# Optimization experiments

Hardware: AMD Instinct MI355X
Metric: run time of the kernel (lower is better)

## Reference

```python
import jax, jax.numpy as jnp
import numpy as np

EPS = 1e-5      # eps used in abs() and log()
BN_EPS = 1e-5   # torch BatchNorm2d default eps


def setup_inputs() -> dict:
    key = jax.random.key(0)
    ks = jax.random.split(key, 5)
    N, C, F, T = 16, 4, 257, 1000
    B, K = 8, 80
    xr = jax.random.normal(ks[0], (N, C, F, T), dtype=jnp.float32)
    xi = jax.random.normal(ks[1], (N, C, F, T), dtype=jnp.float32)
    # per-bin complex beamforming weights: (F, B, C) == Conv1d weight (B*F, 1, C) regrouped
    wr = jax.random.normal(ks[2], (F, B, C), dtype=jnp.float32) * 0.25
    wi = jax.random.normal(ks[3], (F, B, C), dtype=jnp.float32) * 0.25
    # nn.Linear(num_bins, spectra_filters, bias=False) weight: (K, F)
    w_proj = jax.random.normal(ks[4], (K, F), dtype=jnp.float32) * (1.0 / np.sqrt(F))
    gamma = jnp.ones((B,), dtype=jnp.float32)
    beta = jnp.zeros((B,), dtype=jnp.float32)
    return {"xr": xr, "xi": xi, "wr": wr, "wi": wi, "w_proj": w_proj,
            "gamma": gamma, "beta": beta}


def reference(xr, xi, wr, wi, w_proj, gamma, beta):
    # Grouped complex conv1d == per-bin complex beamform across mics:
    # out[n,b,t,f] = sum_c w[f,b,c] * x[n,c,f,t] (complex product)
    br = jnp.einsum('ncft,fbc->nbtf', xr, wr) - jnp.einsum('ncft,fbc->nbtf', xi, wi)
    bi = jnp.einsum('ncft,fbc->nbtf', xi, wr) + jnp.einsum('ncft,fbc->nbtf', xr, wi)
    mag = jnp.sqrt(br * br + bi * bi + EPS)              # (N, B, T, F)
    # Linear(F -> K), ReLU, log
    f = jax.nn.relu(jnp.einsum('nbtf,kf->nbtk', mag, w_proj))
    f = jnp.log(f + EPS)                                  # (N, B, T, K)
    # BatchNorm2d over channel axis B (training-mode batch statistics)
    mean = jnp.mean(f, axis=(0, 2, 3), keepdims=True)
    var = jnp.var(f, axis=(0, 2, 3), keepdims=True)
    f = (f - mean) * jax.lax.rsqrt(var + BN_EPS)
    f = f * gamma[None, :, None, None] + beta[None, :, None, None]
    N, B, T, K = f.shape
    # (N, B, T, K) -> (N, T, B*K)
    return jnp.transpose(f, (0, 2, 1, 3)).reshape(N, T, B * K)
```

## Files before the change

kernel.cpp:

```cpp
#include <hip/hip_runtime.h>
#include <math.h>

#define N_ 16
#define C_ 4
#define F_ 257
#define T_ 1000
#define TP_ 1024
#define B_ 8
#define K_ 80
#define BK_ (B_*K_)

static __device__ __forceinline__ float relu_log(float v) {
    v = fmaxf(v, 0.0f);
    return logf(v + 1e-5f);
}

__global__ __launch_bounds__(256) void k_beamform(
    const float* __restrict__ xr, const float* __restrict__ xi,
    const float* __restrict__ wr, const float* __restrict__ wi,
    float* __restrict__ mag) {
    const int blk = blockIdx.x;
    const int f = blk % F_;
    const int n = blk / F_;

    float wrr[B_][C_], wii[B_][C_];
#pragma unroll
    for (int b = 0; b < B_; ++b)
#pragma unroll
        for (int c = 0; c < C_; ++c) {
            wrr[b][c] = wr[(f * B_ + b) * C_ + c];
            wii[b][c] = wi[(f * B_ + b) * C_ + c];
        }

    const float* xr0 = xr + (size_t)n * C_ * F_ * T_ + (size_t)f * T_;
    const float* xi0 = xi + (size_t)n * C_ * F_ * T_ + (size_t)f * T_;
    float* mag0 = mag + ((size_t)(n * B_) * F_ + f) * TP_;

    for (int t = threadIdx.x; t < TP_; t += 256) {
        if (t < T_) {
            float xrv[C_], xiv[C_];
#pragma unroll
            for (int c = 0; c < C_; ++c) {
                xrv[c] = xr0[(size_t)c * F_ * T_ + t];
                xiv[c] = xi0[(size_t)c * F_ * T_ + t];
            }
#pragma unroll
            for (int b = 0; b < B_; ++b) {
                float br = 0.f, bi = 0.f;
#pragma unroll
                for (int c = 0; c < C_; ++c) {
                    br += xrv[c] * wrr[b][c];
                    br -= xiv[c] * wii[b][c];
                    bi += xiv[c] * wrr[b][c];
                    bi += xrv[c] * wii[b][c];
                }
                float m = sqrtf(br * br + bi * bi + 1e-5f);
                mag0[(size_t)b * F_ * TP_ + t] = m;
            }
        } else {
#pragma unroll
            for (int b = 0; b < B_; ++b)
                mag0[(size_t)b * F_ * TP_ + t] = 0.f;
        }
    }
}

__global__ __launch_bounds__(256) void k_proj(
    const float* __restrict__ mag, const float* __restrict__ w_proj,
    float* __restrict__ out, double* __restrict__ sums) {
    const int bid = blockIdx.x;
    const int tt = bid & 15;
    const int b = (bid >> 4) & 7;
    const int n = bid >> 7;
    const int t0 = tt * 64;

    const int tid = threadIdx.x;
    const int kx = tid & 15;
    const int ty = tid >> 4;
    const int kb = kx * 5;

    __shared__ float magS[32][64];
    __shared__ float wS[32][81];

    float acc[5][4];
#pragma unroll
    for (int j = 0; j < 5; ++j)
#pragma unroll
        for (int i = 0; i < 4; ++i) acc[j][i] = 0.f;

    const float* magNB = mag + ((size_t)(n * B_ + b) * F_) * TP_;

    for (int ch = 0; ch < 8; ++ch) {
        const int f0 = ch * 32;
#pragma unroll
        for (int r = 0; r < 2; ++r) {
            int idx = tid + r * 256;
            int row = idx >> 4, c4 = idx & 15;
            float4 v = *(const float4*)(magNB + (size_t)(f0 + row) * TP_ + t0 + c4 * 4);
            *(float4*)&magS[row][c4 * 4] = v;
        }
#pragma unroll
        for (int r = 0; r < 10; ++r) {
            int idx = tid + r * 256;
            int k = idx >> 5, fc = idx & 31;
            wS[fc][k] = w_proj[k * F_ + f0 + fc];
        }
        __syncthreads();
#pragma unroll 8
        for (int fc = 0; fc < 32; ++fc) {
            float4 m = *(const float4*)&magS[fc][ty * 4];
#pragma unroll
            for (int j = 0; j < 5; ++j) {
                float w = wS[fc][kb + j];
                acc[j][0] += w * m.x;
                acc[j][1] += w * m.y;
                acc[j][2] += w * m.z;
                acc[j][3] += w * m.w;
            }
        }
        __syncthreads();
    }
    {
        float4 m = *(const float4*)(magNB + (size_t)256 * TP_ + t0 + ty * 4);
#pragma unroll
        for (int j = 0; j < 5; ++j) {
            float w = w_proj[(kb + j) * F_ + 256];
            acc[j][0] += w * m.x;
            acc[j][1] += w * m.y;
            acc[j][2] += w * m.z;
            acc[j][3] += w * m.w;
        }
    }

    double s1 = 0.0, s2 = 0.0;
#pragma unroll
    for (int i = 0; i < 4; ++i) {
        int t = t0 + ty * 4 + i;
        if (t < T_) {
            float* orow = out + ((size_t)n * T_ + t) * BK_ + b * K_ + kb;
#pragma unroll
            for (int j = 0; j < 5; ++j) {
                float v = relu_log(acc[j][i]);
                orow[j] = v;
                s1 += (double)v;
                s2 += (double)v * (double)v;
            }
        }
    }
#pragma unroll
    for (int off = 32; off; off >>= 1) {
        s1 += __shfl_down(s1, off);
        s2 += __shfl_down(s2, off);
    }
    __shared__ double red1[4], red2[4];
    int wid = tid >> 6, lane = tid & 63;
    if (lane == 0) { red1[wid] = s1; red2[wid] = s2; }
    __syncthreads();
    if (tid == 0) {
        double a1 = red1[0] + red1[1] + red1[2] + red1[3];
        double a2 = red2[0] + red2[1] + red2[2] + red2[3];
        atomicAdd(&sums[b], a1);
        atomicAdd(&sums[B_ + b], a2);
    }
}

__global__ void k_bnstats(const double* __restrict__ sums,
                          const float* __restrict__ gamma,
                          const float* __restrict__ beta,
                          float* __restrict__ ss) {
    int b = threadIdx.x;
    if (b < B_) {
        const double cnt = (double)N_ * T_ * K_;
        double mean = sums[b] / cnt;
        double var = sums[B_ + b] / cnt - mean * mean;
        float scale = gamma[b] * (float)(1.0 / sqrt(var + 1e-5));
        float shift = beta[b] - (float)mean * scale;
        ss[b] = scale;
        ss[B_ + b] = shift;
    }
}

__global__ __launch_bounds__(256) void k_bnapply(float* __restrict__ out,
                                                 const float* __restrict__ ss) {
    size_t i4 = (size_t)blockIdx.x * 256 + threadIdx.x;
    int k4 = (int)(i4 % (BK_ / 4));
    int b = k4 / (K_ / 4);
    float scale = ss[b], shift = ss[B_ + b];
    float4* p = (float4*)out + i4;
    float4 v = *p;
    v.x = v.x * scale + shift;
    v.y = v.y * scale + shift;
    v.z = v.z * scale + shift;
    v.w = v.w * scale + shift;
    *p = v;
}

extern "C" void kernel_launch(void* const* d_in, const int* in_sizes, int n_in,
                              void* d_out, int out_size, void* d_ws, size_t ws_size,
                              hipStream_t stream) {
    const float* xr = (const float*)d_in[0];
    const float* xi = (const float*)d_in[1];
    const float* wr = (const float*)d_in[2];
    const float* wi = (const float*)d_in[3];
    const float* w_proj = (const float*)d_in[4];
    const float* gamma = (const float*)d_in[5];
    const float* beta = (const float*)d_in[6];
    float* out = (float*)d_out;

    double* sums = (double*)d_ws;
    float* ss = (float*)((char*)d_ws + 128);
    float* mag = (float*)((char*)d_ws + 512);

    hipMemsetAsync(d_ws, 0, 512, stream);
    k_beamform<<<N_ * F_, 256, 0, stream>>>(xr, xi, wr, wi, mag);
    k_proj<<<N_ * B_ * 16, 256, 0, stream>>>(mag, w_proj, out, sums);
    k_bnstats<<<1, 64, 0, stream>>>(sums, gamma, beta, ss);
    k_bnapply<<<10000, 256, 0, stream>>>(out, ss);
}
```

Before: 166.7 us.

## Fuse beamforming into projection kernel, computing magnitudes directly into shared memory

Merges the beamform and projection kernels so each block computes its per-bin magnitudes from the raw complex inputs straight into shared memory, removing the large intermediate magnitude buffer in global memory. The time tile grows to 128 with an 8x5 register tile per thread. The cost is that input spectra are re-read once per beam channel, relying on cache hits, and the grid shrinks, which may lower occupancy.

After: 196.8 us. +18.1%, slower.

```diff
diff --git a/kernel.cpp b/kernel.cpp
--- a/kernel.cpp
+++ b/kernel.cpp
@@ -5,139 +5,162 @@
 #define C_ 4
 #define F_ 257
 #define T_ 1000
-#define TP_ 1024
 #define B_ 8
 #define K_ 80
 #define BK_ (B_*K_)
+#define TT_ 128
 
 static __device__ __forceinline__ float relu_log(float v) {
     v = fmaxf(v, 0.0f);
     return logf(v + 1e-5f);
 }
 
-__global__ __launch_bounds__(256) void k_beamform(
+__global__ __launch_bounds__(256, 4) void k_fused(
     const float* __restrict__ xr, const float* __restrict__ xi,
     const float* __restrict__ wr, const float* __restrict__ wi,
-    float* __restrict__ mag) {
-    const int blk = blockIdx.x;
-    const int f = blk % F_;
-    const int n = blk / F_;
-
-    float wrr[B_][C_], wii[B_][C_];
-#pragma unroll
-    for (int b = 0; b < B_; ++b)
-#pragma unroll
-        for (int c = 0; c < C_; ++c) {
-            wrr[b][c] = wr[(f * B_ + b) * C_ + c];
-            wii[b][c] = wi[(f * B_ + b) * C_ + c];
-        }
-
-    const float* xr0 = xr + (size_t)n * C_ * F_ * T_ + (size_t)f * T_;
-    const float* xi0 = xi + (size_t)n * C_ * F_ * T_ + (size_t)f * T_;
-    float* mag0 = mag + ((size_t)(n * B_) * F_ + f) * TP_;
-
-    for (int t = threadIdx.x; t < TP_; t += 256) {
-        if (t < T_) {
-            float xrv[C_], xiv[C_];
-#pragma unroll
-            for (int c = 0; c < C_; ++c) {
-                xrv[c] = xr0[(size_t)c * F_ * T_ + t];
-                xiv[c] = xi0[(size_t)c * F_ * T_ + t];
-            }
-#pragma unroll
-            for (int b = 0; b < B_; ++b) {
-                float br = 0.f, bi = 0.f;
-#pragma unroll
-                for (int c = 0; c < C_; ++c) {
-                    br += xrv[c] * wrr[b][c];
-                    br -= xiv[c] * wii[b][c];
-                    bi += xiv[c] * wrr[b][c];
-                    bi += xrv[c] * wii[b][c];
-                }
-                float m = sqrtf(br * br + bi * bi + 1e-5f);
-                mag0[(size_t)b * F_ * TP_ + t] = m;
-            }
-        } else {
-#pragma unroll
-            for (int b = 0; b < B_; ++b)
-                mag0[(size_t)b * F_ * TP_ + t] = 0.f;
-        }
-    }
-}
-
-__global__ __launch_bounds__(256) void k_proj(
-    const float* __restrict__ mag, const float* __restrict__ w_proj,
+    const float* __restrict__ w_proj,
     float* __restrict__ out, double* __restrict__ sums) {
+
+    const int tid = threadIdx.x;
     const int bid = blockIdx.x;
-    const int tt = bid & 15;
-    const int b = (bid >> 4) & 7;
-    const int n = bid >> 7;
-    const int t0 = tt * 64;
-
-    const int tid = threadIdx.x;
+    const int b  = bid & 7;
+    const int tt = (bid >> 3) & 7;
+    const int n  = bid >> 6;
+    const int t0 = tt * TT_;
+
+    __shared__ float magS[32][TT_];
+    __shared__ float wS[32][TT_];
+
     const int kx = tid & 15;
     const int ty = tid >> 4;
-    const int kb = kx * 5;
-
-    __shared__ float magS[32][64];
-    __shared__ float wS[32][81];
-
-    float acc[5][4];
+
+    float acc[5][8];
 #pragma unroll
     for (int j = 0; j < 5; ++j)
 #pragma unroll
-        for (int i = 0; i < 4; ++i) acc[j][i] = 0.f;
-
-    const float* magNB = mag + ((size_t)(n * B_ + b) * F_) * TP_;
+        for (int i = 0; i < 8; ++i) acc[j][i] = 0.f;
+
+    const float* xrn = xr + (size_t)n * C_ * F_ * T_;
+    const float* xin = xi + (size_t)n * C_ * F_ * T_;
 
     for (int ch = 0; ch < 8; ++ch) {
         const int f0 = ch * 32;
-#pragma unroll
-        for (int r = 0; r < 2; ++r) {
-            int idx = tid + r * 256;
-            int row = idx >> 4, c4 = idx & 15;
-            float4 v = *(const float4*)(magNB + (size_t)(f0 + row) * TP_ + t0 + c4 * 4);
-            *(float4*)&magS[row][c4 * 4] = v;
-        }
 #pragma unroll
         for (int r = 0; r < 10; ++r) {
             int idx = tid + r * 256;
             int k = idx >> 5, fc = idx & 31;
-            wS[fc][k] = w_proj[k * F_ + f0 + fc];
+            wS[fc][(k / 5) * 8 + (k % 5)] = w_proj[k * F_ + f0 + fc];
+        }
+#pragma unroll
+        for (int r = 0; r < 4; ++r) {
+            int idx = tid + r * 256;
+            int fr = idx >> 5, t4 = idx & 31;
+            int f = f0 + fr;
+            int tb = t0 + t4 * 4;
+            if (tb < T_) {
+                float xrv[C_][4], xiv[C_][4];
+#pragma unroll
+                for (int c = 0; c < C_; ++c) {
+                    float4 vr = *(const float4*)(xrn + ((size_t)c * F_ + f) * T_ + tb);
+                    float4 vi = *(const float4*)(xin + ((size_t)c * F_ + f) * T_ + tb);
+                    xrv[c][0] = vr.x; xrv[c][1] = vr.y; xrv[c][2] = vr.z; xrv[c][3] = vr.w;
+                    xiv[c][0] = vi.x; xiv[c][1] = vi.y; xiv[c][2] = vi.z; xiv[c][3] = vi.w;
+                }
+                float4 wrv = *(const float4*)(wr + (size_t)(f * B_ + b) * C_);
+                float4 wiv = *(const float4*)(wi + (size_t)(f * B_ + b) * C_);
+                float wrc[4] = {wrv.x, wrv.y, wrv.z, wrv.w};
+                float wic[4] = {wiv.x, wiv.y, wiv.z, wiv.w};
+                float4 mres;
+                float* mp = &mres.x;
+#pragma unroll
+                for (int i = 0; i < 4; ++i) {
+                    float br = 0.f, bim = 0.f;
+#pragma unroll
+                    for (int c = 0; c < C_; ++c) {
+                        br  += xrv[c][i] * wrc[c] - xiv[c][i] * wic[c];
+                        bim += xiv[c][i] * wrc[c] + xrv[c][i] * wic[c];
+                    }
+                    mp[i] = sqrtf(br * br + bim * bim + 1e-5f);
+                }
+                *(float4*)&magS[fr][t4 * 4] = mres;
+            } else {
+                *(float4*)&magS[fr][t4 * 4] = make_float4(0.f, 0.f, 0.f, 0.f);
+            }
         }
         __syncthreads();
-#pragma unroll 8
+#pragma unroll 4
         for (int fc = 0; fc < 32; ++fc) {
-            float4 m = *(const float4*)&magS[fc][ty * 4];
-#pragma unroll
-            for (int j = 0; j < 5; ++j) {
-                float w = wS[fc][kb + j];
-                acc[j][0] += w * m.x;
-                acc[j][1] += w * m.y;
-                acc[j][2] += w * m.z;
-                acc[j][3] += w * m.w;
-            }
+            float4 m0 = *(const float4*)&magS[fc][ty * 8];
+            float4 m1 = *(const float4*)&magS[fc][ty * 8 + 4];
+            float4 w0 = *(const float4*)&wS[fc][kx * 8];
+            float  w4 = wS[fc][kx * 8 + 4];
+            float wj[5] = {w0.x, w0.y, w0.z, w0.w, w4};
+            float mi[8] = {m0.x, m0.y, m0.z, m0.w, m1.x, m1.y, m1.z, m1.w};
+#pragma unroll
+            for (int j = 0; j < 5; ++j)
+#pragma unroll
+                for (int i = 0; i < 8; ++i)
+                    acc[j][i] += wj[j] * mi[i];
         }
         __syncthreads();
     }
+
+    if (tid < 80)
+        wS[0][(tid / 5) * 8 + (tid % 5)] = w_proj[tid * F_ + 256];
+    if (tid >= 128 && tid < 160) {
+        int t4 = tid - 128;
+        int tb = t0 + t4 * 4;
+        if (tb < T_) {
+            float xrv[C_][4], xiv[C_][4];
+#pragma unroll
+            for (int c = 0; c < C_; ++c) {
+                float4 vr = *(const float4*)(xrn + ((size_t)c * F_ + 256) * T_ + tb);
+                float4 vi = *(const float4*)(xin + ((size_t)c * F_ + 256) * T_ + tb);
+                xrv[c][0] = vr.x; xrv[c][1] = vr.y; xrv[c][2] = vr.z; xrv[c][3] = vr.w;
+                xiv[c][0] = vi.x; xiv[c][1] = vi.y; xiv[c][2] = vi.z; xiv[c][3] = vi.w;
+            }
+            float4 wrv = *(const float4*)(wr + (size_t)(256 * B_ + b) * C_);
+            float4 wiv = *(const float4*)(wi + (size_t)(256 * B_ + b) * C_);
+            float wrc[4] = {wrv.x, wrv.y, wrv.z, wrv.w};
+            float wic[4] = {wiv.x, wiv.y, wiv.z, wiv.w};
+            float4 mres;
+            float* mp = &mres.x;
+#pragma unroll
+            for (int i = 0; i < 4; ++i) {
+                float br = 0.f, bim = 0.f;
+#pragma unroll
+                for (int c = 0; c < C_; ++c) {
+                    br  += xrv[c][i] * wrc[c] - xiv[c][i] * wic[c];
+                    bim += xiv[c][i] * wrc[c] + xrv[c][i] * wic[c];
+                }
+                mp[i] = sqrtf(br * br + bim * bim + 1e-5f);
+            }
+            *(float4*)&magS[0][t4 * 4] = mres;
+        } else {
+            *(float4*)&magS[0][t4 * 4] = make_float4(0.f, 0.f, 0.f, 0.f);
+        }
+    }
+    __syncthreads();
     {
-        float4 m = *(const float4*)(magNB + (size_t)256 * TP_ + t0 + ty * 4);
-#pragma unroll
-        for (int j = 0; j < 5; ++j) {
-            float w = w_proj[(kb + j) * F_ + 256];
-            acc[j][0] += w * m.x;
-            acc[j][1] += w * m.y;
-            acc[j][2] += w * m.z;
-            acc[j][3] += w * m.w;
-        }
+        float4 m0 = *(const float4*)&magS[0][ty * 8];
+        float4 m1 = *(const float4*)&magS[0][ty * 8 + 4];
+        float4 w0 = *(const float4*)&wS[0][kx * 8];
+        float  w4 = wS[0][kx * 8 + 4];
+        float wj[5] = {w0.x, w0.y, w0.z, w0.w, w4};
+        float mi[8] = {m0.x, m0.y, m0.z, m0.w, m1.x, m1.y, m1.z, m1.w};
+#pragma unroll
+        for (int j = 0; j < 5; ++j)
+#pragma unroll
+            for (int i = 0; i < 8; ++i)
+                acc[j][i] += wj[j] * mi[i];
     }
 
     double s1 = 0.0, s2 = 0.0;
 #pragma unroll
-    for (int i = 0; i < 4; ++i) {
-        int t = t0 + ty * 4 + i;
+    for (int i = 0; i < 8; ++i) {
+        int t = t0 + ty * 8 + i;
         if (t < T_) {
-            float* orow = out + ((size_t)n * T_ + t) * BK_ + b * K_ + kb;
+            float* orow = out + ((size_t)n * T_ + t) * BK_ + b * K_ + kx * 5;
 #pragma unroll
             for (int j = 0; j < 5; ++j) {
                 float v = relu_log(acc[j][i]);
@@ -209,11 +232,9 @@
 
     double* sums = (double*)d_ws;
     float* ss = (float*)((char*)d_ws + 128);
-    float* mag = (float*)((char*)d_ws + 512);
 
     hipMemsetAsync(d_ws, 0, 512, stream);
-    k_beamform<<<N_ * F_, 256, 0, stream>>>(xr, xi, wr, wi, mag);
-    k_proj<<<N_ * B_ * 16, 256, 0, stream>>>(mag, w_proj, out, sums);
+    k_fused<<<N_ * B_ * 8, 256, 0, stream>>>(xr, xi, wr, wi, w_proj, out, sums);
     k_bnstats<<<1, 64, 0, stream>>>(sums, gamma, beta, ss);
     k_bnapply<<<10000, 256, 0, stream>>>(out, ss);
 }
```

## Fuse beamforming into projection kernel and replace atomics with per-block partials

Applied to the files above, without the earlier changes.

Beamforming magnitudes are now computed per 16-frame tile directly into shared memory inside the projection kernel, so the large intermediate magnitude buffer is never written to or read back from global memory. Each block handles all 8 beams for one (n, time-tile), accumulating an 8x5 register tile per thread. BN statistics are written as per-block partial sums reduced by a wider stats kernel, which removes the memset and the double atomics. The cost is that each block recomputes beamforming across all frequencies and holds more registers, and the small 16-frame tiles give lower reuse of the projection weights.

Result: no change. 168.8 us (+1.2%).

```diff
diff --git a/kernel.cpp b/kernel.cpp
--- a/kernel.cpp
+++ b/kernel.cpp
@@ -5,174 +5,224 @@
 #define C_ 4
 #define F_ 257
 #define T_ 1000
-#define TP_ 1024
 #define B_ 8
 #define K_ 80
-#define BK_ (B_*K_)
+#define BK_ 640
+#define TT_ 16
+#define NT_ 63
+#define NBLK (N_ * NT_)
+#define MSTR 260
+#define WSTR 162
 
 static __device__ __forceinline__ float relu_log(float v) {
     v = fmaxf(v, 0.0f);
     return logf(v + 1e-5f);
 }
 
-__global__ __launch_bounds__(256) void k_beamform(
+__global__ __launch_bounds__(256, 3) void k_fused(
     const float* __restrict__ xr, const float* __restrict__ xi,
     const float* __restrict__ wr, const float* __restrict__ wi,
-    float* __restrict__ mag) {
-    const int blk = blockIdx.x;
-    const int f = blk % F_;
-    const int n = blk / F_;
-
-    float wrr[B_][C_], wii[B_][C_];
-#pragma unroll
-    for (int b = 0; b < B_; ++b)
-#pragma unroll
-        for (int c = 0; c < C_; ++c) {
-            wrr[b][c] = wr[(f * B_ + b) * C_ + c];
-            wii[b][c] = wi[(f * B_ + b) * C_ + c];
-        }
-
-    const float* xr0 = xr + (size_t)n * C_ * F_ * T_ + (size_t)f * T_;
-    const float* xi0 = xi + (size_t)n * C_ * F_ * T_ + (size_t)f * T_;
-    float* mag0 = mag + ((size_t)(n * B_) * F_ + f) * TP_;
-
-    for (int t = threadIdx.x; t < TP_; t += 256) {
-        if (t < T_) {
-            float xrv[C_], xiv[C_];
-#pragma unroll
-            for (int c = 0; c < C_; ++c) {
-                xrv[c] = xr0[(size_t)c * F_ * T_ + t];
-                xiv[c] = xi0[(size_t)c * F_ * T_ + t];
-            }
-#pragma unroll
-            for (int b = 0; b < B_; ++b) {
-                float br = 0.f, bi = 0.f;
-#pragma unroll
-                for (int c = 0; c < C_; ++c) {
-                    br += xrv[c] * wrr[b][c];
-                    br -= xiv[c] * wii[b][c];
-                    bi += xiv[c] * wrr[b][c];
-                    bi += xrv[c] * wii[b][c];
-                }
-                float m = sqrtf(br * br + bi * bi + 1e-5f);
-                mag0[(size_t)b * F_ * TP_ + t] = m;
-            }
-        } else {
-#pragma unroll
-            for (int b = 0; b < B_; ++b)
-                mag0[(size_t)b * F_ * TP_ + t] = 0.f;
-        }
-    }
-}
-
-__global__ __launch_bounds__(256) void k_proj(
-    const float* __restrict__ mag, const float* __restrict__ w_proj,
-    float* __restrict__ out, double* __restrict__ sums) {
+    const float* __restrict__ w_proj,
+    float* __restrict__ out, double* __restrict__ partials) {
+
+    const int tid = threadIdx.x;
     const int bid = blockIdx.x;
-    const int tt = bid & 15;
-    const int b = (bid >> 4) & 7;
-    const int n = bid >> 7;
-    const int t0 = tt * 64;
-
-    const int tid = threadIdx.x;
+    const int tt = bid % NT_;
+    const int n  = bid / NT_;
+    const int t0 = tt * TT_;
+
+    __shared__ float magS[TT_][MSTR];
+    __shared__ float wS[32][WSTR];
+    __shared__ double redS[2][4][B_];
+
     const int kx = tid & 15;
     const int ty = tid >> 4;
-    const int kb = kx * 5;
-
-    __shared__ float magS[32][64];
-    __shared__ float wS[32][81];
-
-    float acc[5][4];
-#pragma unroll
-    for (int j = 0; j < 5; ++j)
-#pragma unroll
-        for (int i = 0; i < 4; ++i) acc[j][i] = 0.f;
-
-    const float* magNB = mag + ((size_t)(n * B_ + b) * F_) * TP_;
+
+    const int m_bh = tid & 1;
+    const int m_t4 = (tid >> 1) & 3;
+    const int m_fr = tid >> 3;
+    const int m_b0 = m_bh * 4;
+
+    float acc[B_][5];
+#pragma unroll
+    for (int b = 0; b < B_; ++b)
+#pragma unroll
+        for (int j = 0; j < 5; ++j) acc[b][j] = 0.f;
+
+    const float* xrn = xr + (size_t)n * C_ * F_ * T_;
+    const float* xin = xi + (size_t)n * C_ * F_ * T_;
+    const int kbase = tid >> 5;
+    const int wfc   = tid & 31;
 
     for (int ch = 0; ch < 8; ++ch) {
         const int f0 = ch * 32;
 #pragma unroll
-        for (int r = 0; r < 2; ++r) {
-            int idx = tid + r * 256;
-            int row = idx >> 4, c4 = idx & 15;
-            float4 v = *(const float4*)(magNB + (size_t)(f0 + row) * TP_ + t0 + c4 * 4);
-            *(float4*)&magS[row][c4 * 4] = v;
-        }
-#pragma unroll
         for (int r = 0; r < 10; ++r) {
-            int idx = tid + r * 256;
-            int k = idx >> 5, fc = idx & 31;
-            wS[fc][k] = w_proj[k * F_ + f0 + fc];
+            int k = kbase + 8 * r;
+            wS[wfc][(k / 5) * 10 + (k % 5)] = w_proj[k * F_ + f0 + wfc];
+        }
+        {
+            const int f  = f0 + m_fr;
+            const int tb = t0 + m_t4 * 4;
+            float m[4][4];
+            if (tb + 4 <= T_) {
+                const float* xrp = xrn + (size_t)f * T_ + tb;
+                const float* xip = xin + (size_t)f * T_ + tb;
+                float xrv[C_][4], xiv[C_][4];
+#pragma unroll
+                for (int c = 0; c < C_; ++c) {
+                    float4 vr = *(const float4*)(xrp + (size_t)c * F_ * T_);
+                    float4 vi = *(const float4*)(xip + (size_t)c * F_ * T_);
+                    xrv[c][0] = vr.x; xrv[c][1] = vr.y; xrv[c][2] = vr.z; xrv[c][3] = vr.w;
+                    xiv[c][0] = vi.x; xiv[c][1] = vi.y; xiv[c][2] = vi.z; xiv[c][3] = vi.w;
+                }
+                const float* wrp = wr + (size_t)(f * B_ + m_b0) * C_;
+                const float* wip = wi + (size_t)(f * B_ + m_b0) * C_;
+#pragma unroll
+                for (int jb = 0; jb < 4; ++jb) {
+                    float4 wrv = *(const float4*)(wrp + jb * C_);
+                    float4 wiv = *(const float4*)(wip + jb * C_);
+                    float wrc[4] = {wrv.x, wrv.y, wrv.z, wrv.w};
+                    float wic[4] = {wiv.x, wiv.y, wiv.z, wiv.w};
+#pragma unroll
+                    for (int i = 0; i < 4; ++i) {
+                        float br = 0.f, bi2 = 0.f;
+#pragma unroll
+                        for (int c = 0; c < C_; ++c) {
+                            br  += xrv[c][i] * wrc[c] - xiv[c][i] * wic[c];
+                            bi2 += xiv[c][i] * wrc[c] + xrv[c][i] * wic[c];
+                        }
+                        m[i][jb] = sqrtf(br * br + bi2 * bi2 + 1e-5f);
+                    }
+                }
+            } else {
+#pragma unroll
+                for (int i = 0; i < 4; ++i)
+#pragma unroll
+                    for (int jb = 0; jb < 4; ++jb) m[i][jb] = 0.f;
+            }
+#pragma unroll
+            for (int i = 0; i < 4; ++i)
+                *(float4*)&magS[m_t4 * 4 + i][m_fr * 8 + m_b0] =
+                    make_float4(m[i][0], m[i][1], m[i][2], m[i][3]);
         }
         __syncthreads();
 #pragma unroll 8
         for (int fc = 0; fc < 32; ++fc) {
-            float4 m = *(const float4*)&magS[fc][ty * 4];
+            float4 m0 = *(const float4*)&magS[ty][fc * 8];
+            float4 m1 = *(const float4*)&magS[ty][fc * 8 + 4];
+            float2 wa = *(const float2*)&wS[fc][kx * 10];
+            float2 wb = *(const float2*)&wS[fc][kx * 10 + 2];
+            float  w4 = wS[fc][kx * 10 + 4];
+            float wj[5] = {wa.x, wa.y, wb.x, wb.y, w4};
+            float mb[8] = {m0.x, m0.y, m0.z, m0.w, m1.x, m1.y, m1.z, m1.w};
+#pragma unroll
+            for (int b = 0; b < B_; ++b)
+#pragma unroll
+                for (int j = 0; j < 5; ++j)
+                    acc[b][j] += mb[b] * wj[j];
+        }
+        __syncthreads();
+    }
+
+    if (tid < 80)
+        wS[0][(tid / 5) * 10 + (tid % 5)] = w_proj[tid * F_ + 256];
+    if (tid >= 128) {
+        int id = tid - 128;
+        int trow = id >> 3;
+        int b = id & 7;
+        int t = t0 + trow;
+        float v = 0.f;
+        if (t < T_) {
+            const float* wrp = wr + (size_t)(256 * B_ + b) * C_;
+            const float* wip = wi + (size_t)(256 * B_ + b) * C_;
+            float br = 0.f, bi2 = 0.f;
+#pragma unroll
+            for (int c = 0; c < C_; ++c) {
+                float xrv = xrn[((size_t)c * F_ + 256) * T_ + t];
+                float xiv = xin[((size_t)c * F_ + 256) * T_ + t];
+                br  += xrv * wrp[c] - xiv * wip[c];
+                bi2 += xiv * wrp[c] + xrv * wip[c];
+            }
+            v = sqrtf(br * br + bi2 * bi2 + 1e-5f);
+        }
+        magS[trow][b] = v;
+    }
+    __syncthreads();
+    {
+        float4 m0 = *(const float4*)&magS[ty][0];
+        float4 m1 = *(const float4*)&magS[ty][4];
+        float2 wa = *(const float2*)&wS[0][kx * 10];
+        float2 wb = *(const float2*)&wS[0][kx * 10 + 2];
+        float  w4 = wS[0][kx * 10 + 4];
+        float wj[5] = {wa.x, wa.y, wb.x, wb.y, w4};
+        float mb[8] = {m0.x, m0.y, m0.z, m0.w, m1.x, m1.y, m1.z, m1.w};
+#pragma unroll
+        for (int b = 0; b < B_; ++b)
+#pragma unroll
+            for (int j = 0; j < 5; ++j)
+                acc[b][j] += mb[b] * wj[j];
+    }
+
+    float s1f[B_], s2f[B_];
+#pragma unroll
+    for (int b = 0; b < B_; ++b) { s1f[b] = 0.f; s2f[b] = 0.f; }
+    const int t = t0 + ty;
+    if (t < T_) {
+        float* orow = out + ((size_t)n * T_ + t) * BK_ + kx * 5;
+#pragma unroll
+        for (int b = 0; b < B_; ++b) {
 #pragma unroll
             for (int j = 0; j < 5; ++j) {
-                float w = wS[fc][kb + j];
-                acc[j][0] += w * m.x;
-                acc[j][1] += w * m.y;
-                acc[j][2] += w * m.z;
-                acc[j][3] += w * m.w;
+                float v = relu_log(acc[b][j]);
+                orow[b * K_ + j] = v;
+                s1f[b] += v;
+                s2f[b] += v * v;
             }
         }
-        __syncthreads();
-    }
-    {
-        float4 m = *(const float4*)(magNB + (size_t)256 * TP_ + t0 + ty * 4);
-#pragma unroll
-        for (int j = 0; j < 5; ++j) {
-            float w = w_proj[(kb + j) * F_ + 256];
-            acc[j][0] += w * m.x;
-            acc[j][1] += w * m.y;
-            acc[j][2] += w * m.z;
-            acc[j][3] += w * m.w;
-        }
-    }
-
+    }
+    const int wid = tid >> 6, lane = tid & 63;
+#pragma unroll
+    for (int b = 0; b < B_; ++b) {
+        double d1 = (double)s1f[b], d2 = (double)s2f[b];
+#pragma unroll
+        for (int off = 32; off; off >>= 1) {
+            d1 += __shfl_down(d1, off);
+            d2 += __shfl_down(d2, off);
+        }
+        if (lane == 0) { redS[0][wid][b] = d1; redS[1][wid][b] = d2; }
+    }
+    __syncthreads();
+    if (tid < 8) {
+        partials[(size_t)bid * 16 + tid] =
+            redS[0][0][tid] + redS[0][1][tid] + redS[0][2][tid] + redS[0][3][tid];
+    } else if (tid >= 64 && tid < 72) {
+        int b = tid - 64;
+        partials[(size_t)bid * 16 + 8 + b] =
+            redS[1][0][b] + redS[1][1][b] + redS[1][2][b] + redS[1][3][b];
+    }
+}
+
+__global__ __launch_bounds__(256) void k_bnstats(
+    const double* __restrict__ partials,
+    const float* __restrict__ gamma, const float* __restrict__ beta,
+    float* __restrict__ ss) {
+    const int b = threadIdx.x >> 5;
+    const int i = threadIdx.x & 31;
     double s1 = 0.0, s2 = 0.0;
-#pragma unroll
-    for (int i = 0; i < 4; ++i) {
-        int t = t0 + ty * 4 + i;
-        if (t < T_) {
-            float* orow = out + ((size_t)n * T_ + t) * BK_ + b * K_ + kb;
-#pragma unroll
-            for (int j = 0; j < 5; ++j) {
-                float v = relu_log(acc[j][i]);
-                orow[j] = v;
-                s1 += (double)v;
-                s2 += (double)v * (double)v;
-            }
-        }
-    }
-#pragma unroll
-    for (int off = 32; off; off >>= 1) {
+    for (int j = i; j < NBLK; j += 32) {
+        s1 += partials[(size_t)j * 16 + b];
+        s2 += partials[(size_t)j * 16 + 8 + b];
+    }
+#pragma unroll
+    for (int off = 16; off; off >>= 1) {
         s1 += __shfl_down(s1, off);
         s2 += __shfl_down(s2, off);
     }
-    __shared__ double red1[4], red2[4];
-    int wid = tid >> 6, lane = tid & 63;
-    if (lane == 0) { red1[wid] = s1; red2[wid] = s2; }
-    __syncthreads();
-    if (tid == 0) {
-        double a1 = red1[0] + red1[1] + red1[2] + red1[3];
-        double a2 = red2[0] + red2[1] + red2[2] + red2[3];
-        atomicAdd(&sums[b], a1);
-        atomicAdd(&sums[B_ + b], a2);
-    }
-}
-
-__global__ void k_bnstats(const double* __restrict__ sums,
-                          const float* __restrict__ gamma,
-                          const float* __restrict__ beta,
-                          float* __restrict__ ss) {
-    int b = threadIdx.x;
-    if (b < B_) {
+    if (i == 0) {
         const double cnt = (double)N_ * T_ * K_;
-        double mean = sums[b] / cnt;
-        double var = sums[B_ + b] / cnt - mean * mean;
+        double mean = s1 / cnt;
+        double var = s2 / cnt - mean * mean;
         float scale = gamma[b] * (float)(1.0 / sqrt(var + 1e-5));
         float shift = beta[b] - (float)mean * scale;
         ss[b] = scale;
@@ -207,13 +257,10 @@
     const float* beta = (const float*)d_in[6];
     float* out = (float*)d_out;
 
-    double* sums = (double*)d_ws;
-    float* ss = (float*)((char*)d_ws + 128);
-    float* mag = (float*)((char*)d_ws + 512);
-
-    hipMemsetAsync(d_ws, 0, 512, stream);
-    k_beamform<<<N_ * F_, 256, 0, stream>>>(xr, xi, wr, wi, mag);
-    k_proj<<<N_ * B_ * 16, 256, 0, stream>>>(mag, w_proj, out, sums);
-    k_bnstats<<<1, 64, 0, stream>>>(sums, gamma, beta, ss);
+    double* partials = (double*)d_ws;
+    float* ss = (float*)((char*)d_ws + NBLK * 16 * 8 + 64);
+
+    k_fused<<<NBLK, 256, 0, stream>>>(xr, xi, wr, wi, w_proj, out, partials);
+    k_bnstats<<<1, 256, 0, stream>>>(partials, gamma, beta, ss);
     k_bnapply<<<10000, 256, 0, stream>>>(out, ss);
 }
```
